# Performance work log

Measured on AMD Instinct MI355X. Metric: run time of the kernel, lower is better.

The kernel has to match this reference:

```python
import jax, jax.numpy as jnp
import numpy as np

B, N, D, S = 128, 1024, 512, 64
ITERS = 3
EPS = 1e-8


def setup_inputs() -> dict:
    key = jax.random.key(0)
    ks = jax.random.split(key, 10)
    inp = {
        "inputs_pe": jax.random.normal(ks[0], (B, N, D), dtype=jnp.float32),
        "inputs": jax.random.normal(ks[1], (B, N, D), dtype=jnp.float32),
        "slots": jax.random.normal(ks[2], (1, S, D), dtype=jnp.float32),
        "W1": jax.random.normal(ks[3], (D, D), dtype=jnp.float32) * 0.02,
        "b1": jnp.zeros((D,), dtype=jnp.float32),
        "W2": jax.random.normal(ks[4], (D, D), dtype=jnp.float32) * 0.02,
        "b2": jnp.zeros((D,), dtype=jnp.float32),
        "W3": jax.random.normal(ks[5], (D, D), dtype=jnp.float32) * 0.02,
        "b3": jnp.zeros((D,), dtype=jnp.float32),
    }
    return inp


def reference(inputs_pe, inputs, slots, W1, b1, W2, b2, W3, b3):
    b = inputs_pe.shape[0]
    scale = D ** (-0.5)
    # to_k: Linear -> ReLU -> Linear -> ReLU -> Linear (torch Linear: x @ W.T + b)
    h = jax.nn.relu(jnp.einsum('bnd,ed->bne', inputs_pe, W1) + b1)
    h = jax.nn.relu(jnp.einsum('bnd,ed->bne', h, W2) + b2)
    k = jnp.einsum('bnd,ed->bne', h, W3) + b3  # [b, n, d]

    q = jnp.broadcast_to(slots, (b, S, D))  # slots never updated in the loop
    for _ in range(ITERS):
        dots = jnp.einsum('bid,bjd->bij', q, k) * scale  # [b, S, n]
        s_j = dots.sum(axis=2, keepdims=True)            # sum over keys j -> [b, S, 1]
        s_all = dots.sum(axis=(1, 2), keepdims=True)     # total per batch -> [b, 1, 1]
        dots = dots / s_j * s_all
        attn = jax.nn.sigmoid(dots)
        attn2 = attn / (attn.sum(axis=-1, keepdims=True) + EPS)
        updates = jnp.einsum('bjd,bij->bid', inputs, attn2)  # [b, S, d]
    return updates, attn
```

## Files before the change

### kernel.cpp

```cpp
#include <hip/hip_runtime.h>
#include <stdint.h>

#define Bb 128
#define Nn 1024
#define Dd 512
#define Ss 64

constexpr float kScale = 0.044194173824159216f;
constexpr float kEps = 1e-8f;

typedef __bf16 bf16x8 __attribute__((ext_vector_type(8)));
typedef float f32x4 __attribute__((ext_vector_type(4)));
typedef float f32x16 __attribute__((ext_vector_type(16)));
typedef unsigned short ushort8 __attribute__((ext_vector_type(8)));

#define MFMA32 __builtin_amdgcn_mfma_f32_32x32x16_bf16

__device__ inline unsigned short f2bf_rne(float x) {
  unsigned u = __builtin_bit_cast(unsigned, x);
  u += 0x7FFFu + ((u >> 16) & 1u);
  return (unsigned short)(u >> 16);
}
__device__ inline float bf2f(unsigned short h) {
  unsigned u = ((unsigned)h) << 16;
  return __builtin_bit_cast(float, u);
}

__device__ inline void gl_lds16(const void* g, void* l) {
  typedef unsigned int u32;
  auto gp = (u32 __attribute__((address_space(1)))*)(unsigned long long)(uintptr_t)g;
  auto lp = (u32 __attribute__((address_space(3)))*)(unsigned int)(uintptr_t)l;
  __builtin_amdgcn_global_load_lds(gp, lp, 16, 0, 0);
}

__global__ void cast_split_i(const float* __restrict__ in,
                             unsigned short* __restrict__ out, int n8) {
  int i = blockIdx.x * blockDim.x + threadIdx.x;
  const int stride = gridDim.x * blockDim.x;
  for (; i < n8; i += stride) {
    const float4 v0 = ((const float4*)in)[i * 2];
    const float4 v1 = ((const float4*)in)[i * 2 + 1];
    float f[8] = {v0.x, v0.y, v0.z, v0.w, v1.x, v1.y, v1.z, v1.w};
    ushort8 h, lo;
#pragma unroll
    for (int j = 0; j < 8; j++) {
      h[j] = f2bf_rne(f[j]);
      lo[j] = f2bf_rne(f[j] - bf2f(h[j]));
    }
    ((ushort8*)out)[i * 2] = h;
    ((ushort8*)out)[i * 2 + 1] = lo;
  }
}

template <int ACT>
__global__ __launch_bounds__(256, 2) void gemm_tp(
    const unsigned short* __restrict__ A, const unsigned short* __restrict__ W,
    const float* __restrict__ bias, unsigned short* __restrict__ C) {
  constexpr int NH = 32;
  extern __shared__ unsigned short lds[];
  const int t = threadIdx.x, l = t & 63, w = t >> 6;
  const int wr = w >> 1, wc = w & 1;

  const int wg = ((blockIdx.x & 7) << 9) + (blockIdx.x >> 3);
  const long rowA0 = (long)(wg >> 2) * 128;
  const int colB0 = (wg & 3) * 128;

  const unsigned short* pbase =
      (w < 2) ? A + rowA0 * 1024 : W + (long)colB0 * 1024;
  const int qs = (l & 3) ^ ((l >> 3) & 3);
  const unsigned short* srcp[4];
  int dstp[4];
#pragma unroll
  for (int j = 0; j < 4; j++) {
    const int cid = w * 4 + j;
    const int rloc = (cid & 7) * 16 + (l >> 2);
    srcp[j] = pbase + (long)rloc * 1024 + qs * 8;
    dstp[j] = cid * 512;
  }
#define STG(h)                                                            \
  {                                                                       \
    unsigned short* bq_ = lds + ((h) & 3) * 8192;                         \
    _Pragma("unroll") for (int j = 0; j < 4; j++)                         \
        gl_lds16(srcp[j] + (h) * 32, bq_ + dstp[j]);                      \
  }

  const int ppA = ((2 * (l >> 5)) ^ ((l >> 1) & 3)) * 8;
  const int ar = (wr * 64 + (l & 31)) * 32 + ppA;
  const int br = 4096 + (wc * 64 + (l & 31)) * 32 + ppA;

#define READF(h, S)                                                       \
  {                                                                       \
    const unsigned short* bq_ = lds + ((h) & 3) * 8192;                   \
    _Pragma("unroll") for (int m = 0; m < 2; m++) {                       \
      ah##S[m] = *(const bf16x8*)(bq_ + (ar + m * 1024));                 \
      al##S[m] = *(const bf16x8*)(bq_ + ((ar + m * 1024) ^ 8));           \
    }                                                                     \
    _Pragma("unroll") for (int n = 0; n < 2; n++) {                       \
      bh##S[n] = *(const bf16x8*)(bq_ + (br + n * 1024));                 \
      bl##S[n] = *(const bf16x8*)(bq_ + ((br + n * 1024) ^ 8));           \
    }                                                                     \
  }

#define MFMACL(S)                                                         \
  {                                                                       \
    _Pragma("unroll") for (int m = 0; m < 2; m++)                         \
        _Pragma("unroll") for (int n = 0; n < 2; n++) {                   \
      acc[m][n] = MFMA32(ah##S[m], bh##S[n], acc[m][n], 0, 0, 0);         \
      acc[m][n] = MFMA32(al##S[m], bh##S[n], acc[m][n], 0, 0, 0);         \
      acc[m][n] = MFMA32(ah##S[m], bl##S[n], acc[m][n], 0, 0, 0);         \
    }                                                                     \
  }

#define BODY(h, CUR, NXT)                                                 \
  {                                                                       \
    asm volatile("s_waitcnt lgkmcnt(0)" ::: "memory");                    \
    __builtin_amdgcn_sched_barrier(0);                                    \
    if ((h) < 29) {                                                       \
      asm volatile("s_waitcnt vmcnt(8)" ::: "memory");                    \
    } else if ((h) == 29) {                                               \
      asm volatile("s_waitcnt vmcnt(4)" ::: "memory");                    \
    } else if ((h) == 30) {                                               \
      asm volatile("s_waitcnt vmcnt(0)" ::: "memory");                    \
    }                                                                     \
    __builtin_amdgcn_s_barrier();                                         \
    if ((h) + 4 < NH) STG((h) + 4);                                       \
    if ((h) + 1 < NH) READF((h) + 1, NXT);                                \
    __builtin_amdgcn_sched_barrier(0);                                    \
    __builtin_amdgcn_s_setprio(1);                                        \
    MFMACL(CUR);                                                          \
    __builtin_amdgcn_s_setprio(0);                                        \
  }

  f32x16 acc[2][2] = {};
  bf16x8 ahA[2], alA[2], bhA[2], blA[2];
  bf16x8 ahB[2], alB[2], bhB[2], blB[2];

  STG(0); STG(1); STG(2); STG(3);
  asm volatile("s_waitcnt vmcnt(12)" ::: "memory");
  __builtin_amdgcn_s_barrier();
  READF(0, A);

  for (int hh = 0; hh < NH; hh += 2) {
    BODY(hh, A, B);
    BODY(hh + 1, B, A);
  }
#undef STG
#undef READF
#undef MFMACL
#undef BODY

#pragma unroll
  for (int m = 0; m < 2; m++)
#pragma unroll
    for (int n = 0; n < 2; n++) {
      const int col = colB0 + wc * 64 + n * 32 + (l & 31);
      const float bv = bias[col];
      const int cofs = (col >> 3) * 16 + (col & 7);
#pragma unroll
      for (int r = 0; r < 16; r++) {
        const long row = rowA0 + wr * 64 + m * 32 + (r & 3) + 8 * (r >> 2) + 4 * (l >> 5);
        float xv = acc[m][n][r] + bv;
        if (ACT) xv = fmaxf(xv, 0.0f);
        const unsigned short h = f2bf_rne(xv);
        unsigned short* cp = C + row * 1024 + cofs;
        cp[0] = h;
        cp[8] = f2bf_rne(xv - bf2f(h));
      }
    }
}

__global__ __launch_bounds__(256) void gemm_dots_split(
    const unsigned short* __restrict__ QI, const unsigned short* __restrict__ KI,
    float* __restrict__ dots) {
  constexpr int K = 512, BM = 64, BN = 128, BK = 32;
  __shared__ __align__(16) unsigned short lah[BM * BK];
  __shared__ __align__(16) unsigned short lal[BM * BK];
  __shared__ __align__(16) unsigned short lbh[BN * BK];
  __shared__ __align__(16) unsigned short lbl[BN * BK];
  const int t = threadIdx.x, l = t & 63, w = t >> 6;
  const int b = blockIdx.x >> 3, bc = blockIdx.x & 7;
  const unsigned short* kb = KI + (long)b * Nn * 1024;
  f32x4 acc[4][2] = {};

  const int qbase = (t >> 2) * 1024 + (t & 3) * 16;
  const long kbase0 = (long)(bc * BN + (t >> 2)) * 1024 + (t & 3) * 16;
  const long kbase1 = (long)(bc * BN + 64 + (t >> 2)) * 1024 + (t & 3) * 16;

  for (int k0 = 0; k0 < K; k0 += BK) {
    const int ko = k0 * 2;
    const int lo = w * 512;
    gl_lds16(QI + qbase + ko, lah + lo);
    gl_lds16(QI + qbase + ko + 8, lal + lo);
    gl_lds16(kb + kbase0 + ko, lbh + lo);
    gl_lds16(kb + kbase0 + ko + 8, lbl + lo);
    gl_lds16(kb + kbase1 + ko, lbh + 2048 + lo);
    gl_lds16(kb + kbase1 + ko + 8, lbl + 2048 + lo);
    __syncthreads();
    bf16x8 ah[4], al[4], bh[2], bl[2];
#pragma unroll
    for (int m = 0; m < 4; m++) {
      const int off = (m * 16 + (l & 15)) * BK + (l >> 4) * 8;
      ah[m] = *(const bf16x8*)(lah + off);
      al[m] = *(const bf16x8*)(lal + off);
    }
#pragma unroll
    for (int n = 0; n < 2; n++) {
      const int off = (w * 32 + n * 16 + (l & 15)) * BK + (l >> 4) * 8;
      bh[n] = *(const bf16x8*)(lbh + off);
      bl[n] = *(const bf16x8*)(lbl + off);
    }
#pragma unroll
    for (int m = 0; m < 4; m++)
#pragma unroll
      for (int n = 0; n < 2; n++) {
        acc[m][n] = __builtin_amdgcn_mfma_f32_16x16x32_bf16(ah[m], bh[n], acc[m][n], 0, 0, 0);
        acc[m][n] = __builtin_amdgcn_mfma_f32_16x16x32_bf16(al[m], bh[n], acc[m][n], 0, 0, 0);
        acc[m][n] = __builtin_amdgcn_mfma_f32_16x16x32_bf16(ah[m], bl[n], acc[m][n], 0, 0, 0);
      }
    __syncthreads();
  }
  float* dp = dots + (long)b * Ss * Nn;
#pragma unroll
  for (int m = 0; m < 4; m++) {
    const int row = m * 16 + (l >> 4) * 4;
#pragma unroll
    for (int n = 0; n < 2; n++) {
      const int col = bc * BN + w * 32 + n * 16 + (l & 15);
#pragma unroll
      for (int r = 0; r < 4; r++) dp[(long)(row + r) * Nn + col] = acc[m][n][r] * kScale;
    }
  }
}

__global__ __launch_bounds__(256) void reduce_k(
    const float* __restrict__ dots, float* __restrict__ s_j, float* __restrict__ s_all) {
  const int b = blockIdx.x, t = threadIdx.x, l = t & 63, w = t >> 6;
  const float4* dp = (const float4*)(dots + (long)b * Ss * Nn);
  __shared__ float rowacc[64][4];
  __shared__ float rowsum[64];
  for (int r = 0; r < 64; ++r) {
    const float4 v = dp[r * 256 + t];
    float s = v.x + v.y + v.z + v.w;
#pragma unroll
    for (int off = 32; off; off >>= 1) s += __shfl_down(s, off);
    if (l == 0) rowacc[r][w] = s;
  }
  __syncthreads();
  if (t < 64) {
    const float v = rowacc[t][0] + rowacc[t][1] + rowacc[t][2] + rowacc[t][3];
    rowsum[t] = v;
    s_j[b * 64 + t] = v;
  }
  __syncthreads();
  if (t < 64) {
    float v = rowsum[t];
#pragma unroll
    for (int off = 32; off; off >>= 1) v += __shfl_down(v, off);
    if (t == 0) s_all[b] = v;
  }
}

__global__ __launch_bounds__(256) void attn_k(
    const float* __restrict__ dots, const float* __restrict__ s_j,
    const float* __restrict__ s_all, float* __restrict__ attn_out,
    float* __restrict__ inv_r) {
  const int bi = blockIdx.x;
  const int b = bi >> 6;
  const int t = threadIdx.x;
  const float ratio = s_all[b] / s_j[bi];
  const float* dp = dots + (long)bi * Nn;
  float* ap = attn_out + (long)bi * Nn;
  float s = 0.f;
#pragma unroll
  for (int qq = 0; qq < 4; qq++) {
    const int j = qq * 256 + t;
    const float x = dp[j] * ratio;
    const float a = 1.f / (1.f + expf(-x));
    ap[j] = a;
    s += a;
  }
  __shared__ float red[256];
  red[t] = s;
  __syncthreads();
  for (int off = 128; off > 0; off >>= 1) {
    if (t < off) red[t] += red[t + off];
    __syncthreads();
  }
  if (t == 0) inv_r[bi] = 1.f / (red[0] + kEps);
}

__global__ __launch_bounds__(256) void updates_k3(
    const float* __restrict__ attn, const float* __restrict__ inputs,
    const float* __restrict__ inv_r, float* __restrict__ out0) {
  constexpr int NT2 = 64;
  constexpr int BUF_F = 3072;
  extern __shared__ float ldsf[];
  const int t = threadIdx.x, l = t & 63, w = t >> 6;
  const int b = blockIdx.x >> 2, dt = blockIdx.x & 3;
  const int ig = t >> 5, dg = t & 31;
  const float* inb = inputs + (size_t)b * (Nn * Dd) + dt * 128;
  const float* attsrc = attn + (size_t)b * (Ss * Nn) + (size_t)(t >> 2) * Nn + (t & 3) * 4;
  float acc[8][4] = {};
  float4 ga, gb;

#define UISSUE(bufi, tile, G)                                             \
  {                                                                       \
    const int j0_ = (tile)*16;                                            \
    G = *(const float4*)(attsrc + j0_);                                   \
    float* db_ = ldsf + (bufi)*BUF_F;                                     \
    _Pragma("unroll") for (int i_ = 0; i_ < 2; i_++) {                    \
      const int rb_ = i_ * 8 + w * 2;                                     \
      gl_lds16(inb + (size_t)(j0_ + rb_ + (l >> 5)) * Dd + (l & 31) * 4,  \
               db_ + rb_ * 128);                                          \
    }                                                                     \
  }

#define UWRITE(bufi, G)                                                   \
  {                                                                       \
    float* ab_ = ldsf + (bufi)*BUF_F + 2048;                              \
    const int col_ = t >> 2;                                              \
    const int r0_ = (t & 3) * 4;                                          \
    ab_[(r0_ + 0) * 64 + col_] = G.x;                                     \
    ab_[(r0_ + 1) * 64 + col_] = G.y;                                     \
    ab_[(r0_ + 2) * 64 + col_] = G.z;                                     \
    ab_[(r0_ + 3) * 64 + col_] = G.w;                                     \
  }

#define UCOMP(bufi)                                                       \
  {                                                                       \
    const float* db_ = ldsf + (bufi)*BUF_F;                               \
    const float* ab_ = db_ + 2048;                                        \
    _Pragma("unroll 4") for (int jj = 0; jj < 16; jj++) {                 \
      float av[8], vv[4];                                                 \
      *(float4*)&av[0] = *(const float4*)(ab_ + jj * 64 + ig * 8);        \
      *(float4*)&av[4] = *(const float4*)(ab_ + jj * 64 + ig * 8 + 4);    \
      *(float4*)&vv[0] = *(const float4*)(db_ + jj * 128 + dg * 4);       \
      _Pragma("unroll") for (int m_ = 0; m_ < 8; m_++)                    \
          _Pragma("unroll") for (int n_ = 0; n_ < 4; n_++)                \
              acc[m_][n_] = __builtin_fmaf(av[m_], vv[n_], acc[m_][n_]);  \
    }                                                                     \
  }

  UISSUE(0, 0, ga);
  UISSUE(1, 1, gb);
  UWRITE(0, ga);

  for (int tt = 0; tt < NT2; tt += 2) {
    asm volatile("s_waitcnt vmcnt(3)" ::: "memory");
    UWRITE((tt + 1) % 3, gb);
    asm volatile("s_waitcnt lgkmcnt(0)" ::: "memory");
    __builtin_amdgcn_s_barrier();
    __builtin_amdgcn_sched_barrier(0);
    if (tt < NT2 - 2) UISSUE((tt + 2) % 3, tt + 2, ga);
    UCOMP(tt % 3);
    if (tt + 1 < NT2 - 1) {
      asm volatile("s_waitcnt vmcnt(3)" ::: "memory");
    } else {
      asm volatile("s_waitcnt vmcnt(0)" ::: "memory");
    }
    if (tt + 1 < NT2 - 1) UWRITE((tt + 2) % 3, ga);
    asm volatile("s_waitcnt lgkmcnt(0)" ::: "memory");
    __builtin_amdgcn_s_barrier();
    __builtin_amdgcn_sched_barrier(0);
    if (tt + 1 < NT2 - 2) UISSUE((tt + 3) % 3, tt + 3, gb);
    UCOMP((tt + 1) % 3);
  }
#undef UISSUE
#undef UWRITE
#undef UCOMP

#pragma unroll
  for (int m = 0; m < 8; m++) {
    const int i = ig * 8 + m;
    const float ir = inv_r[b * 64 + i];
    float4 o;
    o.x = acc[m][0] * ir; o.y = acc[m][1] * ir; o.z = acc[m][2] * ir; o.w = acc[m][3] * ir;
    float* op = out0 + (size_t)(b * 64 + i) * Dd + dt * 128 + dg * 4;
    *(float4*)op = o;
  }
}

extern "C" void kernel_launch(void* const* d_in, const int* in_sizes, int n_in,
                              void* d_out, int out_size, void* d_ws, size_t ws_size,
                              hipStream_t stream) {
  (void)in_sizes; (void)n_in; (void)out_size; (void)ws_size;
  const float* inputs_pe = (const float*)d_in[0];
  const float* inputs = (const float*)d_in[1];
  const float* slots = (const float*)d_in[2];
  const float* W1 = (const float*)d_in[3];
  const float* b1 = (const float*)d_in[4];
  const float* W2 = (const float*)d_in[5];
  const float* b2 = (const float*)d_in[6];
  const float* W3 = (const float*)d_in[7];
  const float* b3 = (const float*)d_in[8];

  char* ws = (char*)d_ws;
  size_t off = 0;
  auto alloc = [&](size_t bytes) -> void* {
    void* p = ws + off;
    off += (bytes + 255) & ~(size_t)255;
    return p;
  };
  const size_t actB = (size_t)Bb * Nn * 1024 * 2;
  unsigned short* AI = (unsigned short*)alloc(actB);
  unsigned short* BI = (unsigned short*)alloc(actB);
  unsigned short* w1i = (unsigned short*)alloc(Dd * 1024 * 2);
  unsigned short* w2i = (unsigned short*)alloc(Dd * 1024 * 2);
  unsigned short* w3i = (unsigned short*)alloc(Dd * 1024 * 2);
  unsigned short* qi = (unsigned short*)alloc(Ss * 1024 * 2);
  float* dotsb = (float*)alloc((size_t)Bb * Ss * Nn * 4);
  float* s_j = (float*)alloc(Bb * Ss * 4);
  float* s_all = (float*)alloc(Bb * 4);
  float* inv_r = (float*)alloc(Bb * Ss * 4);

  float* out_updates = (float*)d_out;
  float* out_attn = out_updates + (size_t)Bb * Ss * Dd;

  const int kLdsG = 4 * 16 * 1024;
  const int kLdsU = 3 * 12 * 1024;
  hipFuncSetAttribute(reinterpret_cast<const void*>(gemm_tp<1>),
                      hipFuncAttributeMaxDynamicSharedMemorySize, kLdsG);
  hipFuncSetAttribute(reinterpret_cast<const void*>(gemm_tp<0>),
                      hipFuncAttributeMaxDynamicSharedMemorySize, kLdsG);
  hipFuncSetAttribute(reinterpret_cast<const void*>(updates_k3),
                      hipFuncAttributeMaxDynamicSharedMemorySize, kLdsU);

  cast_split_i<<<4096, 256, 0, stream>>>(inputs_pe, AI, Bb * Nn * Dd / 8);
  cast_split_i<<<128, 256, 0, stream>>>(W1, w1i, Dd * Dd / 8);
  cast_split_i<<<128, 256, 0, stream>>>(W2, w2i, Dd * Dd / 8);
  cast_split_i<<<128, 256, 0, stream>>>(W3, w3i, Dd * Dd / 8);
  cast_split_i<<<16, 256, 0, stream>>>(slots, qi, Ss * Dd / 8);

  gemm_tp<1><<<4096, 256, kLdsG, stream>>>(AI, w1i, b1, BI);
  gemm_tp<1><<<4096, 256, kLdsG, stream>>>(BI, w2i, b2, AI);
  gemm_tp<0><<<4096, 256, kLdsG, stream>>>(AI, w3i, b3, BI);

  gemm_dots_split<<<Bb * 8, 256, 0, stream>>>(qi, BI, dotsb);
  reduce_k<<<Bb, 256, 0, stream>>>(dotsb, s_j, s_all);
  attn_k<<<Bb * Ss, 256, 0, stream>>>(dotsb, s_j, s_all, out_attn, inv_r);
  updates_k3<<<Bb * 4, 256, kLdsU, stream>>>(out_attn, inputs, inv_r, out_updates);
}
```

Measured before the change: 1.169 ms.

## Use 8-wave GEMM blocks and widen updates tile to 256 columns

The MLP GEMM now runs 512 threads (8 waves) per 128x128 tile instead of 4. Each wave computes a 64x32 sub-tile and issues two staging loads per K-step instead of four, which adds latency hiding through more waves, and the vmcnt waits are adjusted to match. The updates kernel now covers 256 output columns per block with 8x8 accumulators per thread, halving the grid and the number of times the attention tile is reloaded. The cost is more registers and LDS per block in the updates kernel, and less per-wave MFMA reuse in the GEMM.

```diff
diff --git a/kernel.cpp b/kernel.cpp
--- a/kernel.cpp
+++ b/kernel.cpp
@@ -53,61 +53,60 @@
 }
 
 template <int ACT>
-__global__ __launch_bounds__(256, 2) void gemm_tp(
+__global__ __launch_bounds__(512, 4) void gemm_2b(
     const unsigned short* __restrict__ A, const unsigned short* __restrict__ W,
     const float* __restrict__ bias, unsigned short* __restrict__ C) {
   constexpr int NH = 32;
   extern __shared__ unsigned short lds[];
   const int t = threadIdx.x, l = t & 63, w = t >> 6;
-  const int wr = w >> 1, wc = w & 1;
+  const int wr = w >> 2, wc = w & 3;
 
   const int wg = ((blockIdx.x & 7) << 9) + (blockIdx.x >> 3);
   const long rowA0 = (long)(wg >> 2) * 128;
   const int colB0 = (wg & 3) * 128;
 
-  const unsigned short* pbase =
-      (w < 2) ? A + rowA0 * 1024 : W + (long)colB0 * 1024;
   const int qs = (l & 3) ^ ((l >> 3) & 3);
-  const unsigned short* srcp[4];
-  int dstp[4];
-#pragma unroll
-  for (int j = 0; j < 4; j++) {
-    const int cid = w * 4 + j;
-    const int rloc = (cid & 7) * 16 + (l >> 2);
-    srcp[j] = pbase + (long)rloc * 1024 + qs * 8;
+  const unsigned short* srcp[2];
+  int dstp[2];
+#pragma unroll
+  for (int j = 0; j < 2; j++) {
+    const int cid = w * 2 + j;
+    const unsigned short* base =
+        (cid < 8) ? A + rowA0 * 1024 : W + (long)colB0 * 1024;
+    const int rrel = (cid & 7) * 16 + (l >> 2);
+    srcp[j] = base + (long)rrel * 1024 + qs * 8;
     dstp[j] = cid * 512;
   }
 #define STG(h)                                                            \
   {                                                                       \
     unsigned short* bq_ = lds + ((h) & 3) * 8192;                         \
-    _Pragma("unroll") for (int j = 0; j < 4; j++)                         \
+    _Pragma("unroll") for (int j = 0; j < 2; j++)                         \
         gl_lds16(srcp[j] + (h) * 32, bq_ + dstp[j]);                      \
   }
 
   const int ppA = ((2 * (l >> 5)) ^ ((l >> 1) & 3)) * 8;
-  const int ar = (wr * 64 + (l & 31)) * 32 + ppA;
-  const int br = 4096 + (wc * 64 + (l & 31)) * 32 + ppA;
+  int aoff[2];
+#pragma unroll
+  for (int m = 0; m < 2; m++) aoff[m] = (wr * 64 + m * 32 + (l & 31)) * 32 + ppA;
+  const int boff = 4096 + (wc * 32 + (l & 31)) * 32 + ppA;
 
 #define READF(h, S)                                                       \
   {                                                                       \
     const unsigned short* bq_ = lds + ((h) & 3) * 8192;                   \
     _Pragma("unroll") for (int m = 0; m < 2; m++) {                       \
-      ah##S[m] = *(const bf16x8*)(bq_ + (ar + m * 1024));                 \
-      al##S[m] = *(const bf16x8*)(bq_ + ((ar + m * 1024) ^ 8));           \
+      ah##S[m] = *(const bf16x8*)(bq_ + aoff[m]);                         \
+      al##S[m] = *(const bf16x8*)(bq_ + (aoff[m] ^ 8));                   \
     }                                                                     \
-    _Pragma("unroll") for (int n = 0; n < 2; n++) {                       \
-      bh##S[n] = *(const bf16x8*)(bq_ + (br + n * 1024));                 \
-      bl##S[n] = *(const bf16x8*)(bq_ + ((br + n * 1024) ^ 8));           \
-    }                                                                     \
+    bh##S = *(const bf16x8*)(bq_ + boff);                                 \
+    bl##S = *(const bf16x8*)(bq_ + (boff ^ 8));                           \
   }
 
 #define MFMACL(S)                                                         \
   {                                                                       \
-    _Pragma("unroll") for (int m = 0; m < 2; m++)                         \
-        _Pragma("unroll") for (int n = 0; n < 2; n++) {                   \
-      acc[m][n] = MFMA32(ah##S[m], bh##S[n], acc[m][n], 0, 0, 0);         \
-      acc[m][n] = MFMA32(al##S[m], bh##S[n], acc[m][n], 0, 0, 0);         \
-      acc[m][n] = MFMA32(ah##S[m], bl##S[n], acc[m][n], 0, 0, 0);         \
+    _Pragma("unroll") for (int m = 0; m < 2; m++) {                       \
+      acc[m] = MFMA32(ah##S[m], bh##S, acc[m], 0, 0, 0);                  \
+      acc[m] = MFMA32(al##S[m], bh##S, acc[m], 0, 0, 0);                  \
+      acc[m] = MFMA32(ah##S[m], bl##S, acc[m], 0, 0, 0);                  \
     }                                                                     \
   }
 
@@ -116,9 +115,9 @@
     asm volatile("s_waitcnt lgkmcnt(0)" ::: "memory");                    \
     __builtin_amdgcn_sched_barrier(0);                                    \
     if ((h) < 29) {                                                       \
-      asm volatile("s_waitcnt vmcnt(8)" ::: "memory");                    \
+      asm volatile("s_waitcnt vmcnt(4)" ::: "memory");                    \
     } else if ((h) == 29) {                                               \
-      asm volatile("s_waitcnt vmcnt(4)" ::: "memory");                    \
+      asm volatile("s_waitcnt vmcnt(2)" ::: "memory");                    \
     } else if ((h) == 30) {                                               \
       asm volatile("s_waitcnt vmcnt(0)" ::: "memory");                    \
     }                                                                     \
@@ -131,12 +130,12 @@
     __builtin_amdgcn_s_setprio(0);                                        \
   }
 
-  f32x16 acc[2][2] = {};
-  bf16x8 ahA[2], alA[2], bhA[2], blA[2];
-  bf16x8 ahB[2], alB[2], bhB[2], blB[2];
+  f32x16 acc[2] = {};
+  bf16x8 ahA[2], alA[2], bhA, blA;
+  bf16x8 ahB[2], alB[2], bhB, blB;
 
   STG(0); STG(1); STG(2); STG(3);
-  asm volatile("s_waitcnt vmcnt(12)" ::: "memory");
+  asm volatile("s_waitcnt vmcnt(6)" ::: "memory");
   __builtin_amdgcn_s_barrier();
   READF(0, A);
 
@@ -150,23 +149,21 @@
 #undef BODY
 
 #pragma unroll
-  for (int m = 0; m < 2; m++)
-#pragma unroll
-    for (int n = 0; n < 2; n++) {
-      const int col = colB0 + wc * 64 + n * 32 + (l & 31);
-      const float bv = bias[col];
-      const int cofs = (col >> 3) * 16 + (col & 7);
-#pragma unroll
-      for (int r = 0; r < 16; r++) {
-        const long row = rowA0 + wr * 64 + m * 32 + (r & 3) + 8 * (r >> 2) + 4 * (l >> 5);
-        float xv = acc[m][n][r] + bv;
-        if (ACT) xv = fmaxf(xv, 0.0f);
-        const unsigned short h = f2bf_rne(xv);
-        unsigned short* cp = C + row * 1024 + cofs;
-        cp[0] = h;
-        cp[8] = f2bf_rne(xv - bf2f(h));
-      }
-    }
+  for (int m = 0; m < 2; m++) {
+    const int col = colB0 + wc * 32 + (l & 31);
+    const float bv = bias[col];
+    const int cofs = (col >> 3) * 16 + (col & 7);
+#pragma unroll
+    for (int r = 0; r < 16; r++) {
+      const long row = rowA0 + wr * 64 + m * 32 + (r & 3) + 8 * (r >> 2) + 4 * (l >> 5);
+      float xv = acc[m][r] + bv;
+      if (ACT) xv = fmaxf(xv, 0.0f);
+      const unsigned short h = f2bf_rne(xv);
+      unsigned short* cp = C + row * 1024 + cofs;
+      cp[0] = h;
+      cp[8] = f2bf_rne(xv - bf2f(h));
+    }
+  }
 }
 
 __global__ __launch_bounds__(256) void gemm_dots_split(
@@ -289,18 +286,18 @@
   if (t == 0) inv_r[bi] = 1.f / (red[0] + kEps);
 }
 
-__global__ __launch_bounds__(256) void updates_k3(
+__global__ __launch_bounds__(256) void updates_k5(
     const float* __restrict__ attn, const float* __restrict__ inputs,
     const float* __restrict__ inv_r, float* __restrict__ out0) {
   constexpr int NT2 = 64;
-  constexpr int BUF_F = 3072;
+  constexpr int BUF_F = 5120;
   extern __shared__ float ldsf[];
-  const int t = threadIdx.x, l = t & 63, w = t >> 6;
-  const int b = blockIdx.x >> 2, dt = blockIdx.x & 3;
+  const int t = threadIdx.x, lam = t & 63, w = t >> 6;
+  const int b = blockIdx.x >> 1, dt = blockIdx.x & 1;
   const int ig = t >> 5, dg = t & 31;
-  const float* inb = inputs + (size_t)b * (Nn * Dd) + dt * 128;
+  const float* inb = inputs + (size_t)b * (Nn * Dd) + dt * 256;
   const float* attsrc = attn + (size_t)b * (Ss * Nn) + (size_t)(t >> 2) * Nn + (t & 3) * 4;
-  float acc[8][4] = {};
+  float acc[8][8] = {};
   float4 ga, gb;
 
 #define UISSUE(bufi, tile, G)                                             \
@@ -308,16 +305,15 @@
     const int j0_ = (tile)*16;                                            \
     G = *(const float4*)(attsrc + j0_);                                   \
     float* db_ = ldsf + (bufi)*BUF_F;                                     \
-    _Pragma("unroll") for (int i_ = 0; i_ < 2; i_++) {                    \
-      const int rb_ = i_ * 8 + w * 2;                                     \
-      gl_lds16(inb + (size_t)(j0_ + rb_ + (l >> 5)) * Dd + (l & 31) * 4,  \
-               db_ + rb_ * 128);                                          \
+    _Pragma("unroll") for (int i_ = 0; i_ < 4; i_++) {                    \
+      const int row_ = i_ * 4 + w;                                        \
+      gl_lds16(inb + (size_t)(j0_ + row_) * Dd + lam * 4, db_ + row_ * 256); \
     }                                                                     \
   }
 
 #define UWRITE(bufi, G)                                                   \
   {                                                                       \
-    float* ab_ = ldsf + (bufi)*BUF_F + 2048;                              \
+    float* ab_ = ldsf + (bufi)*BUF_F + 4096;                              \
     const int col_ = t >> 2;                                              \
     const int r0_ = (t & 3) * 4;                                          \
     ab_[(r0_ + 0) * 64 + col_] = G.x;                                     \
@@ -329,14 +325,15 @@
 #define UCOMP(bufi)                                                       \
   {                                                                       \
     const float* db_ = ldsf + (bufi)*BUF_F;                               \
-    const float* ab_ = db_ + 2048;                                        \
+    const float* ab_ = db_ + 4096;                                        \
     _Pragma("unroll 4") for (int jj = 0; jj < 16; jj++) {                 \
-      float av[8], vv[4];                                                 \
+      float av[8], vv[8];                                                 \
       *(float4*)&av[0] = *(const float4*)(ab_ + jj * 64 + ig * 8);        \
       *(float4*)&av[4] = *(const float4*)(ab_ + jj * 64 + ig * 8 + 4);    \
-      *(float4*)&vv[0] = *(const float4*)(db_ + jj * 128 + dg * 4);       \
+      *(float4*)&vv[0] = *(const float4*)(db_ + jj * 256 + dg * 8);       \
+      *(float4*)&vv[4] = *(const float4*)(db_ + jj * 256 + dg * 8 + 4);   \
       _Pragma("unroll") for (int m_ = 0; m_ < 8; m_++)                    \
-          _Pragma("unroll") for (int n_ = 0; n_ < 4; n_++)                \
+          _Pragma("unroll") for (int n_ = 0; n_ < 8; n_++)                \
               acc[m_][n_] = __builtin_fmaf(av[m_], vv[n_], acc[m_][n_]);  \
     }                                                                     \
   }
@@ -346,7 +343,7 @@
   UWRITE(0, ga);
 
   for (int tt = 0; tt < NT2; tt += 2) {
-    asm volatile("s_waitcnt vmcnt(3)" ::: "memory");
+    asm volatile("s_waitcnt vmcnt(5)" ::: "memory");
     UWRITE((tt + 1) % 3, gb);
     asm volatile("s_waitcnt lgkmcnt(0)" ::: "memory");
     __builtin_amdgcn_s_barrier();
@@ -354,7 +351,7 @@
     if (tt < NT2 - 2) UISSUE((tt + 2) % 3, tt + 2, ga);
     UCOMP(tt % 3);
     if (tt + 1 < NT2 - 1) {
-      asm volatile("s_waitcnt vmcnt(3)" ::: "memory");
+      asm volatile("s_waitcnt vmcnt(5)" ::: "memory");
     } else {
       asm volatile("s_waitcnt vmcnt(0)" ::: "memory");
     }
@@ -373,10 +370,12 @@
   for (int m = 0; m < 8; m++) {
     const int i = ig * 8 + m;
     const float ir = inv_r[b * 64 + i];
-    float4 o;
-    o.x = acc[m][0] * ir; o.y = acc[m][1] * ir; o.z = acc[m][2] * ir; o.w = acc[m][3] * ir;
-    float* op = out0 + (size_t)(b * 64 + i) * Dd + dt * 128 + dg * 4;
-    *(float4*)op = o;
+    float4 o0, o1;
+    o0.x = acc[m][0] * ir; o0.y = acc[m][1] * ir; o0.z = acc[m][2] * ir; o0.w = acc[m][3] * ir;
+    o1.x = acc[m][4] * ir; o1.y = acc[m][5] * ir; o1.z = acc[m][6] * ir; o1.w = acc[m][7] * ir;
+    float* op = out0 + (size_t)(b * 64 + i) * Dd + dt * 256 + dg * 8;
+    *(float4*)op = o0;
+    *(float4*)(op + 4) = o1;
   }
 }
 
@@ -417,12 +416,12 @@
   float* out_attn = out_updates + (size_t)Bb * Ss * Dd;
 
   const int kLdsG = 4 * 16 * 1024;
-  const int kLdsU = 3 * 12 * 1024;
-  hipFuncSetAttribute(reinterpret_cast<const void*>(gemm_tp<1>),
+  const int kLdsU = 3 * 20 * 1024;
+  hipFuncSetAttribute(reinterpret_cast<const void*>(gemm_2b<1>),
                       hipFuncAttributeMaxDynamicSharedMemorySize, kLdsG);
-  hipFuncSetAttribute(reinterpret_cast<const void*>(gemm_tp<0>),
+  hipFuncSetAttribute(reinterpret_cast<const void*>(gemm_2b<0>),
                       hipFuncAttributeMaxDynamicSharedMemorySize, kLdsG);
-  hipFuncSetAttribute(reinterpret_cast<const void*>(updates_k3),
+  hipFuncSetAttribute(reinterpret_cast<const void*>(updates_k5),
                       hipFuncAttributeMaxDynamicSharedMemorySize, kLdsU);
 
   cast_split_i<<<4096, 256, 0, stream>>>(inputs_pe, AI, Bb * Nn * Dd / 8);
@@ -431,12 +430,12 @@
   cast_split_i<<<128, 256, 0, stream>>>(W3, w3i, Dd * Dd / 8);
   cast_split_i<<<16, 256, 0, stream>>>(slots, qi, Ss * Dd / 8);
 
-  gemm_tp<1><<<4096, 256, kLdsG, stream>>>(AI, w1i, b1, BI);
-  gemm_tp<1><<<4096, 256, kLdsG, stream>>>(BI, w2i, b2, AI);
-  gemm_tp<0><<<4096, 256, kLdsG, stream>>>(AI, w3i, b3, BI);
+  gemm_2b<1><<<4096, 512, kLdsG, stream>>>(AI, w1i, b1, BI);
+  gemm_2b<1><<<4096, 512, kLdsG, stream>>>(BI, w2i, b2, AI);
+  gemm_2b<0><<<4096, 512, kLdsG, stream>>>(AI, w3i, b3, BI);
 
   gemm_dots_split<<<Bb * 8, 256, 0, stream>>>(qi, BI, dotsb);
   reduce_k<<<Bb, 256, 0, stream>>>(dotsb, s_j, s_all);
   attn_k<<<Bb * Ss, 256, 0, stream>>>(dotsb, s_j, s_all, out_attn, inv_r);
-  updates_k3<<<Bb * 4, 256, kLdsU, stream>>>(out_attn, inputs, inv_r, out_updates);
-}
+  updates_k5<<<Bb * 2, 256, kLdsU, stream>>>(out_attn, inputs, inv_r, out_updates);
+}
```

Result: no change. 1.184 ms (+1.3%).
